# Performance work log

Hardware: AMD Instinct MI355X
Metric: run time of the kernel (lower is better)

The kernel has to match this reference:

```python
import jax, jax.numpy as jnp
import numpy as np

H = 1024          # hidden_size
NE = 16           # num_experts
GS = 4            # group_size (experts sharing a down projection)
DFF = int(H * 4 * 2 / 3)  # 2730, int(hidden*ffn_dim_multiplier*ffn_ratio)
BATCH, SEQ = 4, 2048
BS = BATCH * SEQ  # 8192 flattened tokens


def setup_inputs() -> dict:
    key = jax.random.key(0)
    k1, k2, k3, k4 = jax.random.split(key, 4)
    return {
        "x": jax.random.normal(k1, (BS, H), dtype=jnp.float32),
        "router_w": jax.random.normal(k2, (H, NE), dtype=jnp.float32) * 0.02,
        "router_b": jnp.zeros((NE,), dtype=jnp.float32),
        "up_w": jax.random.normal(k3, (NE, H, DFF), dtype=jnp.float32) * 0.02,
        "up_b": jnp.zeros((NE, DFF), dtype=jnp.float32),
        "down_w": jax.random.normal(k4, (NE // GS, DFF, H), dtype=jnp.float32) * 0.02,
        "down_b": jnp.zeros((NE // GS, H), dtype=jnp.float32),
        "batch_size": BATCH,
        "seq_len": SEQ,
    }


def reference(x, router_w, router_b, up_w, up_b, down_w, down_b, batch_size, seq_len):
    bs, hidden = x.shape
    num_experts = router_w.shape[1]
    # expert-choice capacity: k = bs * c // num_experts with c = 1.0
    k = bs // num_experts

    # linear router
    h_logits = x @ router_w + router_b          # [bs, E]
    S = jax.nn.softmax(h_logits, axis=-1)       # [bs, E]

    # each expert picks its top-k tokens (torch.topk(S, k, dim=0))
    G, idx = jax.lax.top_k(S.T, k)               # G: [E, k], idx: [E, k]

    # dispatch: einsum('bs k e, bs h -> e k h', P, x) == gather of chosen tokens
    tokens = x[idx]                              # [E, k, H]

    # grouped per-expert FFN: experts in a group share the down projection
    group_size = num_experts // down_w.shape[0]
    dw = jnp.repeat(down_w, group_size, axis=0)  # [E, DFF, H]
    db = jnp.repeat(down_b, group_size, axis=0)  # [E, H]

    hid = jax.nn.silu(jnp.einsum('ekh,ehd->ekd', tokens, up_w) + up_b[:, None, :])
    E_out = jnp.einsum('ekd,edh->ekh', hid, dw) + db[:, None, :]  # [E, k, H]

    # combine: einsum('bs k e, k e, e k h -> bs h', P, G, E) == weighted scatter-add
    weighted = G[:, :, None] * E_out             # [E, k, H]
    y = jnp.zeros_like(x).at[idx.reshape(-1)].add(weighted.reshape(-1, hidden))
    return y
```

## Files before the change

kernel.cpp:

```cpp
#include <hip/hip_runtime.h>
#include <stdint.h>

#define H 1024
#define NE 16
#define DFF 2730
#define DFFP 2752
#define DFFT 2816
#define BS 8192
#define KSEL 512
#define LDSP 40

typedef unsigned short u16;
typedef __attribute__((ext_vector_type(8))) short short8;
typedef __attribute__((ext_vector_type(4))) float f32x4;

__device__ __forceinline__ u16 f2b(float f) {
  unsigned u = __float_as_uint(f);
  unsigned r = (u + 0x7fffu + ((u >> 16) & 1u)) >> 16;
  return (u16)r;
}

__global__ __launch_bounds__(256) void zero_kernel(f32x4* __restrict__ out) {
  size_t i = ((size_t)blockIdx.x * 256 + threadIdx.x) * 2;
  f32x4 z = {0.f, 0.f, 0.f, 0.f};
  out[i] = z; out[i + 1] = z;
}

__global__ __launch_bounds__(256) void transcvt_kernel(
    const float* __restrict__ src, u16* __restrict__ dst,
    int Ks, int Ns, int Kd, long src_z, long dst_z) {
  src += (size_t)blockIdx.z * src_z;
  dst += (size_t)blockIdx.z * dst_z;
  __shared__ float t[32][33];
  int k0 = blockIdx.x * 32, n0 = blockIdx.y * 32;
  int r = threadIdx.x >> 3, c4 = (threadIdx.x & 7) * 4;
  int k = k0 + r;
#pragma unroll
  for (int j = 0; j < 4; ++j) {
    int n = n0 + c4 + j;
    t[r][c4 + j] = (k < Ks && n < Ns) ? src[(size_t)k * Ns + n] : 0.f;
  }
  __syncthreads();
  u16 o[4];
#pragma unroll
  for (int j = 0; j < 4; ++j) o[j] = f2b(t[c4 + j][r]);
  *(uint2*)&dst[(size_t)(n0 + r) * Kd + k0 + c4] = *(uint2*)o;
}

__global__ __launch_bounds__(256) void router_kernel(
    const float* __restrict__ x, const float* __restrict__ rw,
    const float* __restrict__ rb, double* __restrict__ S64, float* __restrict__ S32) {
  int w = threadIdx.x >> 6, lane = threadIdx.x & 63;
  int t = blockIdx.x * 4 + w;
  __shared__ double part[4][64][17];
  double acc[NE];
#pragma unroll
  for (int e = 0; e < NE; ++e) acc[e] = 0.0;
  const float* xr = x + (size_t)t * H + lane * 16;
  f32x4 xv[4];
#pragma unroll
  for (int q = 0; q < 4; ++q) xv[q] = *(const f32x4*)(xr + q * 4);
#pragma unroll
  for (int hh = 0; hh < 16; ++hh) {
    double xf = (double)xv[hh >> 2][hh & 3];
    const float* rwr = rw + (size_t)(lane * 16 + hh) * NE;
    f32x4 wv0 = *(const f32x4*)rwr;
    f32x4 wv1 = *(const f32x4*)(rwr + 4);
    f32x4 wv2 = *(const f32x4*)(rwr + 8);
    f32x4 wv3 = *(const f32x4*)(rwr + 12);
#pragma unroll
    for (int e = 0; e < 4; ++e) acc[e]      += xf * (double)wv0[e];
#pragma unroll
    for (int e = 0; e < 4; ++e) acc[4 + e]  += xf * (double)wv1[e];
#pragma unroll
    for (int e = 0; e < 4; ++e) acc[8 + e]  += xf * (double)wv2[e];
#pragma unroll
    for (int e = 0; e < 4; ++e) acc[12 + e] += xf * (double)wv3[e];
  }
#pragma unroll
  for (int e = 0; e < NE; ++e) part[w][lane][e] = acc[e];
  __syncthreads();
  if (lane < NE) {
    double s = (double)rb[lane];
#pragma unroll 8
    for (int r = 0; r < 64; ++r) s += part[w][r][lane];
    double m = s;
    for (int o = 8; o > 0; o >>= 1) m = fmax(m, __shfl_xor(m, o, 16));
    double ex = exp(s - m);
    double sum = ex;
    for (int o = 8; o > 0; o >>= 1) sum += __shfl_xor(sum, o, 16);
    double Sv = ex / sum;
    S64[(size_t)lane * BS + t] = Sv;
    S32[(size_t)lane * BS + t] = (float)Sv;
  }
}

__global__ __launch_bounds__(256) void topk_kernel(
    const float* __restrict__ S32, const double* __restrict__ S64,
    int* __restrict__ sel, float* __restrict__ gates) {
  int e = blockIdx.x, tid = threadIdx.x;
  __shared__ float sv[BS];
  __shared__ int red[4];
  __shared__ int cnt_s, gt_s, tie_cnt;
  __shared__ int tie_idx[256];
  const float* row = S32 + (size_t)e * BS;
  for (int i = tid; i < BS; i += 256) sv[i] = row[i];
  if (tid == 0) tie_cnt = 0;
  __syncthreads();
  unsigned thr = 0;
  for (int bit = 31; bit >= 0; --bit) {
    unsigned cand = thr | (1u << bit);
    int c = 0;
    for (int i = tid; i < BS; i += 256) c += (__float_as_uint(sv[i]) >= cand) ? 1 : 0;
#pragma unroll
    for (int o = 32; o > 0; o >>= 1) c += __shfl_down(c, o);
    if ((tid & 63) == 0) red[tid >> 6] = c;
    __syncthreads();
    if (tid == 0) cnt_s = red[0] + red[1] + red[2] + red[3];
    __syncthreads();
    if (cnt_s >= KSEL) thr = cand;
    __syncthreads();
  }
  {
    int c = 0;
    for (int i = tid; i < BS; i += 256) c += (__float_as_uint(sv[i]) > thr) ? 1 : 0;
#pragma unroll
    for (int o = 32; o > 0; o >>= 1) c += __shfl_down(c, o);
    if ((tid & 63) == 0) red[tid >> 6] = c;
    __syncthreads();
    if (tid == 0) gt_s = red[0] + red[1] + red[2] + red[3];
    __syncthreads();
  }
  int gt = gt_s;
  if (tid < 64) {
    int lane = tid, pos = 0;
    for (int c = 0; c < BS / 64; ++c) {
      int i = c * 64 + lane;
      bool p = __float_as_uint(sv[i]) > thr;
      unsigned long long b = __ballot(p);
      int rank = __popcll(b & ((1ull << lane) - 1ull));
      if (p) { sel[e * KSEL + pos + rank] = i; gates[e * KSEL + pos + rank] = sv[i]; }
      pos += __popcll(b);
    }
  }
  for (int i = tid; i < BS; i += 256) {
    if (__float_as_uint(sv[i]) == thr) {
      int p = atomicAdd(&tie_cnt, 1);
      if (p < 256) tie_idx[p] = i;
    }
  }
  __syncthreads();
  int T = tie_cnt < 256 ? tie_cnt : 256;
  int R = KSEL - gt;
  if (tid < T) {
    int i = tie_idx[tid];
    double vi = S64[(size_t)e * BS + i];
    int rank = 0;
    for (int j = 0; j < T; ++j) {
      if (j == tid) continue;
      int kdx = tie_idx[j];
      double vj = S64[(size_t)e * BS + kdx];
      rank += (vj > vi || (vj == vi && kdx < i)) ? 1 : 0;
    }
    if (rank < R) {
      sel[e * KSEL + gt + rank] = i;
      gates[e * KSEL + gt + rank] = sv[i];
    }
  }
}

__global__ __launch_bounds__(256) void up_gemm_kernel(
    const float* __restrict__ x, const int* __restrict__ sel,
    const u16* __restrict__ upT, const float* __restrict__ up_b,
    u16* __restrict__ hid, int e_base) {
  int nt = blockIdx.x;
  int mt = blockIdx.y;
  int z = blockIdx.z;
  int e = e_base + z;
  const u16* upTz = upT + (size_t)z * DFFT * H;
  u16* hidz = hid + (size_t)z * KSEL * DFFP;
  int tid = threadIdx.x, lane = tid & 63, w = tid >> 6;
  int wm = (w >> 1) * 64, wn = (w & 1) * 64;
  int n0 = nt * 128, m0 = mt * 128;
  __shared__ u16 As[128][LDSP];
  __shared__ u16 Bs[128][LDSP];
  __shared__ int sel_s[128];
  if (tid < 128) sel_s[tid] = sel[e * KSEL + m0 + tid];
  f32x4 zero = {0.f, 0.f, 0.f, 0.f};
  f32x4 acc[4][4];
#pragma unroll
  for (int i = 0; i < 4; ++i)
#pragma unroll
    for (int j = 0; j < 4; ++j) acc[i][j] = zero;
  int bn = tid & 127, bq = tid >> 7;
  const u16* brow = upTz + (size_t)(n0 + bn) * H + bq * 16;
  int arow = tid >> 1, ahalf = tid & 1;
  __syncthreads();
  const float* xrow = x + (size_t)sel_s[arow] * H + ahalf * 16;
  for (int k0 = 0; k0 < H; k0 += 32) {
    const float* ap = xrow + k0;
    f32x4 a0 = *(const f32x4*)ap;
    f32x4 a1 = *(const f32x4*)(ap + 4);
    f32x4 a2 = *(const f32x4*)(ap + 8);
    f32x4 a3 = *(const f32x4*)(ap + 12);
    short8 pa0, pa1;
#pragma unroll
    for (int q = 0; q < 4; ++q) { pa0[q] = (short)f2b(a0[q]); pa0[4 + q] = (short)f2b(a1[q]); }
#pragma unroll
    for (int q = 0; q < 4; ++q) { pa1[q] = (short)f2b(a2[q]); pa1[4 + q] = (short)f2b(a3[q]); }
    short8 qb0 = *(const short8*)(brow + k0);
    short8 qb1 = *(const short8*)(brow + k0 + 8);
    __syncthreads();
    *(short8*)&As[arow][ahalf * 16] = pa0;
    *(short8*)&As[arow][ahalf * 16 + 8] = pa1;
    *(short8*)&Bs[bn][bq * 16] = qb0;
    *(short8*)&Bs[bn][bq * 16 + 8] = qb1;
    __syncthreads();
    int lm = lane & 15, lk = (lane >> 4) * 8;
    short8 af[4], bfr[4];
#pragma unroll
    for (int i = 0; i < 4; ++i) af[i] = *(short8*)&As[wm + i * 16 + lm][lk];
#pragma unroll
    for (int j = 0; j < 4; ++j) bfr[j] = *(short8*)&Bs[wn + j * 16 + lm][lk];
#pragma unroll
    for (int i = 0; i < 4; ++i)
#pragma unroll
      for (int j = 0; j < 4; ++j)
        acc[i][j] = __builtin_amdgcn_mfma_f32_16x16x32_bf16(af[i], bfr[j], acc[i][j], 0, 0, 0);
  }
  int lm = lane & 15, q = lane >> 4;
#pragma unroll
  for (int i = 0; i < 4; ++i) {
#pragma unroll
    for (int j = 0; j < 4; ++j) {
      int col = n0 + wn + j * 16 + lm;
      if (col >= DFFP) continue;
      float bias = (col < DFF) ? up_b[(size_t)e * DFF + col] : 0.f;
#pragma unroll
      for (int r = 0; r < 4; ++r) {
        int rowl = m0 + wm + i * 16 + q * 4 + r;
        float v = acc[i][j][r] + bias;
        v = v / (1.f + __expf(-v));
        hidz[(size_t)rowl * DFFP + col] = f2b(v);
      }
    }
  }
}

__global__ __launch_bounds__(256) void down_gemm_kernel(
    const u16* __restrict__ hid, const u16* __restrict__ dwT,
    const float* __restrict__ db, const int* __restrict__ selp,
    const float* __restrict__ gatesp, float* __restrict__ out) {
  int nt = blockIdx.x;
  int mt = blockIdx.y;
  int z = blockIdx.z;
  const u16* hidz = hid + (size_t)z * 2048 * DFFP;
  const u16* dwTz = dwT + (size_t)z * H * DFFP;
  const float* dbz = db + (size_t)z * H;
  const int* selz = selp + z * 2048;
  const float* gatesz = gatesp + z * 2048;
  int tid = threadIdx.x, lane = tid & 63, w = tid >> 6;
  int wm = (w >> 1) * 64, wn = (w & 1) * 64;
  int n0 = nt * 128, m0 = mt * 128;
  __shared__ u16 As[128][LDSP];
  __shared__ u16 Bs[128][LDSP];
  __shared__ int sel_s[128];
  __shared__ float gate_s[128];
  if (tid < 128) {
    sel_s[tid] = selz[m0 + tid];
    gate_s[tid] = gatesz[m0 + tid];
  }
  f32x4 zero = {0.f, 0.f, 0.f, 0.f};
  f32x4 acc[4][4];
#pragma unroll
  for (int i = 0; i < 4; ++i)
#pragma unroll
    for (int j = 0; j < 4; ++j) acc[i][j] = zero;
  int bn = tid & 127, bq = tid >> 7;
  const u16* brow = dwTz + (size_t)(n0 + bn) * DFFP + bq * 16;
  int arow0 = tid >> 2, akv = tid & 3;
  __syncthreads();
  for (int k0 = 0; k0 < DFFP; k0 += 32) {
    short8 av0 = *(const short8*)(hidz + (size_t)(m0 + arow0) * DFFP + k0 + akv * 8);
    short8 av1 = *(const short8*)(hidz + (size_t)(m0 + arow0 + 64) * DFFP + k0 + akv * 8);
    short8 qb0 = *(const short8*)(brow + k0);
    short8 qb1 = *(const short8*)(brow + k0 + 8);
    __syncthreads();
    *(short8*)&As[arow0][akv * 8] = av0;
    *(short8*)&As[arow0 + 64][akv * 8] = av1;
    *(short8*)&Bs[bn][bq * 16] = qb0;
    *(short8*)&Bs[bn][bq * 16 + 8] = qb1;
    __syncthreads();
    int lm = lane & 15, lk = (lane >> 4) * 8;
    short8 af[4], bfr[4];
#pragma unroll
    for (int i = 0; i < 4; ++i) af[i] = *(short8*)&As[wm + i * 16 + lm][lk];
#pragma unroll
    for (int j = 0; j < 4; ++j) bfr[j] = *(short8*)&Bs[wn + j * 16 + lm][lk];
#pragma unroll
    for (int i = 0; i < 4; ++i)
#pragma unroll
      for (int j = 0; j < 4; ++j)
        acc[i][j] = __builtin_amdgcn_mfma_f32_16x16x32_bf16(af[i], bfr[j], acc[i][j], 0, 0, 0);
  }
  int lm = lane & 15, q = lane >> 4;
#pragma unroll
  for (int i = 0; i < 4; ++i) {
#pragma unroll
    for (int j = 0; j < 4; ++j) {
      int col = n0 + wn + j * 16 + lm;
      float bias = dbz[col];
#pragma unroll
      for (int r = 0; r < 4; ++r) {
        int rowl = wm + i * 16 + q * 4 + r;
        float v = (acc[i][j][r] + bias) * gate_s[rowl];
        atomicAdd(&out[(size_t)sel_s[rowl] * H + col], v);
      }
    }
  }
}

extern "C" void kernel_launch(void* const* d_in, const int* in_sizes, int n_in,
                              void* d_out, int out_size, void* d_ws, size_t ws_size,
                              hipStream_t stream) {
  const float* x      = (const float*)d_in[0];
  const float* rw     = (const float*)d_in[1];
  const float* rb     = (const float*)d_in[2];
  const float* up_w   = (const float*)d_in[3];
  const float* up_b   = (const float*)d_in[4];
  const float* down_w = (const float*)d_in[5];
  const float* down_b = (const float*)d_in[6];
  char* ws = (char*)d_ws;
  double* S64  = (double*)ws;
  float*  S32  = (float*)(ws + 1048576);
  int*    sel  = (int*)(ws + 1572864);
  float*  gates= (float*)(ws + 1605632);
  const size_t base = 1638400;

  const size_t upT_e  = (size_t)DFFT * H * 2;
  const size_t dwT_g  = (size_t)H * DFFP * 2;
  const size_t hid_e  = (size_t)KSEL * DFFP * 2;

  size_t need16 = base + 16 * upT_e + 4 * dwT_g + 16 * hid_e;
  size_t need4  = base + 4 * upT_e + 1 * dwT_g + 4 * hid_e;
  int cs = (ws_size >= need16) ? 16 : (ws_size >= need4 ? 4 : 1);

  float* outf = (float*)d_out;
  zero_kernel<<<BS * H / 8 / 256, 256, 0, stream>>>((f32x4*)d_out);
  router_kernel<<<BS / 4, 256, 0, stream>>>(x, rw, rb, S64, S32);
  topk_kernel<<<NE, 256, 0, stream>>>(S32, S64, sel, gates);

  if (cs == 16) {
    u16* upT = (u16*)(ws + base);
    u16* dwT = (u16*)(ws + base + 16 * upT_e);
    u16* hid = (u16*)(ws + base + 16 * upT_e + 4 * dwT_g);
    transcvt_kernel<<<dim3(H / 32, DFFT / 32, 16), 256, 0, stream>>>(
        up_w, upT, H, DFF, H, (long)H * DFF, (long)DFFT * H);
    transcvt_kernel<<<dim3(DFFP / 32, H / 32, 4), 256, 0, stream>>>(
        down_w, dwT, DFF, H, DFFP, (long)DFF * H, (long)H * DFFP);
    up_gemm_kernel<<<dim3(22, 4, 16), 256, 0, stream>>>(x, sel, upT, up_b, hid, 0);
    down_gemm_kernel<<<dim3(8, 16, 4), 256, 0, stream>>>(hid, dwT, down_b, sel, gates, outf);
  } else if (cs == 4) {
    u16* upT = (u16*)(ws + base);
    u16* dwT = (u16*)(ws + base + 4 * upT_e);
    u16* hid = (u16*)(ws + base + 4 * upT_e + dwT_g);
    for (int g = 0; g < 4; ++g) {
      transcvt_kernel<<<dim3(H / 32, DFFT / 32, 4), 256, 0, stream>>>(
          up_w + (size_t)g * 4 * H * DFF, upT, H, DFF, H, (long)H * DFF, (long)DFFT * H);
      transcvt_kernel<<<dim3(DFFP / 32, H / 32, 1), 256, 0, stream>>>(
          down_w + (size_t)g * DFF * H, dwT, DFF, H, DFFP, 0, 0);
      up_gemm_kernel<<<dim3(22, 4, 4), 256, 0, stream>>>(x, sel, upT, up_b, hid, g * 4);
      down_gemm_kernel<<<dim3(8, 16, 1), 256, 0, stream>>>(
          hid, dwT, down_b + g * H, sel + g * 2048, gates + g * 2048, outf);
    }
  } else {
    u16* upT = (u16*)(ws + base);
    u16* dwT = (u16*)(ws + base + upT_e);
    u16* hid = (u16*)(ws + base + upT_e + dwT_g);
    for (int e = 0; e < 16; ++e) {
      transcvt_kernel<<<dim3(H / 32, DFFT / 32, 1), 256, 0, stream>>>(
          up_w + (size_t)e * H * DFF, upT, H, DFF, H, 0, 0);
      transcvt_kernel<<<dim3(DFFP / 32, H / 32, 1), 256, 0, stream>>>(
          down_w + (size_t)(e >> 2) * DFF * H, dwT, DFF, H, DFFP, 0, 0);
      up_gemm_kernel<<<dim3(22, 4, 1), 256, 0, stream>>>(x, sel, upT, up_b, hid, e);
      down_gemm_kernel<<<dim3(8, 4, 1), 256, 0, stream>>>(
          hid, dwT, down_b + (e >> 2) * H, sel + e * KSEL, gates + e * KSEL, outf);
    }
  }
}
```

Measured before the change: 705.6 us.

## Pre-gather bf16 tokens and load GEMM tiles directly to LDS with swizzle

Adds a gather kernel that converts the selected token rows to bf16 once, so the up GEMM no longer re-reads and re-converts fp32 x for every N tile. Both GEMMs now fill shared memory with global_load_lds, store tiles unpadded with an XOR swizzle to avoid bank conflicts, and swap the grid axes so blocks sharing a weight tile launch together. This cuts register staging and redundant conversion, but costs an extra launch and workspace for the gathered tokens, and the loop still uses single-buffered loads with two barriers per step.

```diff
diff --git a/kernel.cpp b/kernel.cpp
--- a/kernel.cpp
+++ b/kernel.cpp
@@ -8,7 +8,6 @@
 #define DFFT 2816
 #define BS 8192
 #define KSEL 512
-#define LDSP 40
 
 typedef unsigned short u16;
 typedef __attribute__((ext_vector_type(8))) short short8;
@@ -18,6 +17,12 @@
   unsigned u = __float_as_uint(f);
   unsigned r = (u + 0x7fffu + ((u >> 16) & 1u)) >> 16;
   return (u16)r;
+}
+
+typedef const __attribute__((address_space(1))) unsigned int* gas_t;
+typedef __attribute__((address_space(3))) unsigned int* las_t;
+__device__ __forceinline__ void gload16(const u16* g, u16* l) {
+  __builtin_amdgcn_global_load_lds((gas_t)g, (las_t)l, 16, 0, 0);
 }
 
 __global__ __launch_bounds__(256) void zero_kernel(f32x4* __restrict__ out) {
@@ -45,6 +50,17 @@
 #pragma unroll
   for (int j = 0; j < 4; ++j) o[j] = f2b(t[c4 + j][r]);
   *(uint2*)&dst[(size_t)(n0 + r) * Kd + k0 + c4] = *(uint2*)o;
+}
+
+__global__ __launch_bounds__(256) void gather_kernel(
+    const float* __restrict__ x, const int* __restrict__ sel, u16* __restrict__ xg) {
+  int row = blockIdx.x;
+  const float* src = x + (size_t)sel[row] * H + threadIdx.x * 4;
+  f32x4 v = *(const f32x4*)src;
+  u16 o[4];
+#pragma unroll
+  for (int j = 0; j < 4; ++j) o[j] = f2b(v[j]);
+  *(uint2*)&xg[(size_t)row * H + threadIdx.x * 4] = *(uint2*)o;
 }
 
 __global__ __launch_bounds__(256) void router_kernel(
@@ -169,66 +185,61 @@
   }
 }
 
+
 __global__ __launch_bounds__(256) void up_gemm_kernel(
-    const float* __restrict__ x, const int* __restrict__ sel,
-    const u16* __restrict__ upT, const float* __restrict__ up_b,
-    u16* __restrict__ hid, int e_base) {
-  int nt = blockIdx.x;
-  int mt = blockIdx.y;
+    const u16* __restrict__ xg, const u16* __restrict__ upT,
+    const float* __restrict__ up_b, u16* __restrict__ hid, int e_base) {
+  int mt = blockIdx.x;
+  int nt = blockIdx.y;
   int z = blockIdx.z;
   int e = e_base + z;
-  const u16* upTz = upT + (size_t)z * DFFT * H;
+  const u16* Abase = xg + (size_t)z * KSEL * H + (size_t)(mt * 128) * H;
+  const u16* Bbase = upT + (size_t)z * DFFT * H + (size_t)(nt * 128) * H;
   u16* hidz = hid + (size_t)z * KSEL * DFFP;
   int tid = threadIdx.x, lane = tid & 63, w = tid >> 6;
   int wm = (w >> 1) * 64, wn = (w & 1) * 64;
   int n0 = nt * 128, m0 = mt * 128;
-  __shared__ u16 As[128][LDSP];
-  __shared__ u16 Bs[128][LDSP];
-  __shared__ int sel_s[128];
-  if (tid < 128) sel_s[tid] = sel[e * KSEL + m0 + tid];
+  __shared__ __align__(16) u16 As[128 * 32];
+  __shared__ __align__(16) u16 Bs[128 * 32];
+  int r0 = tid >> 2, cg0 = (tid & 3) ^ ((r0 >> 1) & 3);
+  const u16* pa0 = Abase + (size_t)r0 * H + cg0 * 8;
+  const u16* pa1 = Abase + (size_t)(r0 + 64) * H + cg0 * 8;
+  const u16* pb0 = Bbase + (size_t)r0 * H + cg0 * 8;
+  const u16* pb1 = Bbase + (size_t)(r0 + 64) * H + cg0 * 8;
+  u16* la0 = As + tid * 8;  u16* la1 = As + 2048 + tid * 8;
+  u16* lb0 = Bs + tid * 8;  u16* lb1 = Bs + 2048 + tid * 8;
   f32x4 zero = {0.f, 0.f, 0.f, 0.f};
   f32x4 acc[4][4];
 #pragma unroll
   for (int i = 0; i < 4; ++i)
 #pragma unroll
     for (int j = 0; j < 4; ++j) acc[i][j] = zero;
-  int bn = tid & 127, bq = tid >> 7;
-  const u16* brow = upTz + (size_t)(n0 + bn) * H + bq * 16;
-  int arow = tid >> 1, ahalf = tid & 1;
-  __syncthreads();
-  const float* xrow = x + (size_t)sel_s[arow] * H + ahalf * 16;
+  int lm = lane & 15, g = lane >> 4;
   for (int k0 = 0; k0 < H; k0 += 32) {
-    const float* ap = xrow + k0;
-    f32x4 a0 = *(const f32x4*)ap;
-    f32x4 a1 = *(const f32x4*)(ap + 4);
-    f32x4 a2 = *(const f32x4*)(ap + 8);
-    f32x4 a3 = *(const f32x4*)(ap + 12);
-    short8 pa0, pa1;
-#pragma unroll
-    for (int q = 0; q < 4; ++q) { pa0[q] = (short)f2b(a0[q]); pa0[4 + q] = (short)f2b(a1[q]); }
-#pragma unroll
-    for (int q = 0; q < 4; ++q) { pa1[q] = (short)f2b(a2[q]); pa1[4 + q] = (short)f2b(a3[q]); }
-    short8 qb0 = *(const short8*)(brow + k0);
-    short8 qb1 = *(const short8*)(brow + k0 + 8);
-    __syncthreads();
-    *(short8*)&As[arow][ahalf * 16] = pa0;
-    *(short8*)&As[arow][ahalf * 16 + 8] = pa1;
-    *(short8*)&Bs[bn][bq * 16] = qb0;
-    *(short8*)&Bs[bn][bq * 16 + 8] = qb1;
-    __syncthreads();
-    int lm = lane & 15, lk = (lane >> 4) * 8;
+    gload16(pa0 + k0, la0);
+    gload16(pa1 + k0, la1);
+    gload16(pb0 + k0, lb0);
+    gload16(pb1 + k0, lb1);
+    __syncthreads();
     short8 af[4], bfr[4];
 #pragma unroll
-    for (int i = 0; i < 4; ++i) af[i] = *(short8*)&As[wm + i * 16 + lm][lk];
-#pragma unroll
-    for (int j = 0; j < 4; ++j) bfr[j] = *(short8*)&Bs[wn + j * 16 + lm][lk];
+    for (int i = 0; i < 4; ++i) {
+      int row = wm + i * 16 + lm;
+      af[i] = *(short8*)&As[row * 32 + ((g ^ ((row >> 1) & 3)) * 8)];
+    }
+#pragma unroll
+    for (int j = 0; j < 4; ++j) {
+      int row = wn + j * 16 + lm;
+      bfr[j] = *(short8*)&Bs[row * 32 + ((g ^ ((row >> 1) & 3)) * 8)];
+    }
 #pragma unroll
     for (int i = 0; i < 4; ++i)
 #pragma unroll
       for (int j = 0; j < 4; ++j)
         acc[i][j] = __builtin_amdgcn_mfma_f32_16x16x32_bf16(af[i], bfr[j], acc[i][j], 0, 0, 0);
-  }
-  int lm = lane & 15, q = lane >> 4;
+    __syncthreads();
+  }
+  int q = lane >> 4;
 #pragma unroll
   for (int i = 0; i < 4; ++i) {
 #pragma unroll
@@ -251,59 +262,63 @@
     const u16* __restrict__ hid, const u16* __restrict__ dwT,
     const float* __restrict__ db, const int* __restrict__ selp,
     const float* __restrict__ gatesp, float* __restrict__ out) {
-  int nt = blockIdx.x;
-  int mt = blockIdx.y;
+  int mt = blockIdx.x;
+  int nt = blockIdx.y;
   int z = blockIdx.z;
-  const u16* hidz = hid + (size_t)z * 2048 * DFFP;
-  const u16* dwTz = dwT + (size_t)z * H * DFFP;
+  const u16* Abase = hid + (size_t)z * 2048 * DFFP + (size_t)(mt * 128) * DFFP;
+  const u16* Bbase = dwT + (size_t)z * H * DFFP + (size_t)(nt * 128) * DFFP;
   const float* dbz = db + (size_t)z * H;
-  const int* selz = selp + z * 2048;
-  const float* gatesz = gatesp + z * 2048;
   int tid = threadIdx.x, lane = tid & 63, w = tid >> 6;
   int wm = (w >> 1) * 64, wn = (w & 1) * 64;
   int n0 = nt * 128, m0 = mt * 128;
-  __shared__ u16 As[128][LDSP];
-  __shared__ u16 Bs[128][LDSP];
+  __shared__ __align__(16) u16 As[128 * 32];
+  __shared__ __align__(16) u16 Bs[128 * 32];
   __shared__ int sel_s[128];
   __shared__ float gate_s[128];
   if (tid < 128) {
-    sel_s[tid] = selz[m0 + tid];
-    gate_s[tid] = gatesz[m0 + tid];
-  }
+    sel_s[tid] = selp[z * 2048 + m0 + tid];
+    gate_s[tid] = gatesp[z * 2048 + m0 + tid];
+  }
+  int r0 = tid >> 2, cg0 = (tid & 3) ^ ((r0 >> 1) & 3);
+  const u16* pa0 = Abase + (size_t)r0 * DFFP + cg0 * 8;
+  const u16* pa1 = Abase + (size_t)(r0 + 64) * DFFP + cg0 * 8;
+  const u16* pb0 = Bbase + (size_t)r0 * DFFP + cg0 * 8;
+  const u16* pb1 = Bbase + (size_t)(r0 + 64) * DFFP + cg0 * 8;
+  u16* la0 = As + tid * 8;  u16* la1 = As + 2048 + tid * 8;
+  u16* lb0 = Bs + tid * 8;  u16* lb1 = Bs + 2048 + tid * 8;
   f32x4 zero = {0.f, 0.f, 0.f, 0.f};
   f32x4 acc[4][4];
 #pragma unroll
   for (int i = 0; i < 4; ++i)
 #pragma unroll
     for (int j = 0; j < 4; ++j) acc[i][j] = zero;
-  int bn = tid & 127, bq = tid >> 7;
-  const u16* brow = dwTz + (size_t)(n0 + bn) * DFFP + bq * 16;
-  int arow0 = tid >> 2, akv = tid & 3;
+  int lm = lane & 15, g = lane >> 4;
   __syncthreads();
   for (int k0 = 0; k0 < DFFP; k0 += 32) {
-    short8 av0 = *(const short8*)(hidz + (size_t)(m0 + arow0) * DFFP + k0 + akv * 8);
-    short8 av1 = *(const short8*)(hidz + (size_t)(m0 + arow0 + 64) * DFFP + k0 + akv * 8);
-    short8 qb0 = *(const short8*)(brow + k0);
-    short8 qb1 = *(const short8*)(brow + k0 + 8);
-    __syncthreads();
-    *(short8*)&As[arow0][akv * 8] = av0;
-    *(short8*)&As[arow0 + 64][akv * 8] = av1;
-    *(short8*)&Bs[bn][bq * 16] = qb0;
-    *(short8*)&Bs[bn][bq * 16 + 8] = qb1;
-    __syncthreads();
-    int lm = lane & 15, lk = (lane >> 4) * 8;
+    gload16(pa0 + k0, la0);
+    gload16(pa1 + k0, la1);
+    gload16(pb0 + k0, lb0);
+    gload16(pb1 + k0, lb1);
+    __syncthreads();
     short8 af[4], bfr[4];
 #pragma unroll
-    for (int i = 0; i < 4; ++i) af[i] = *(short8*)&As[wm + i * 16 + lm][lk];
-#pragma unroll
-    for (int j = 0; j < 4; ++j) bfr[j] = *(short8*)&Bs[wn + j * 16 + lm][lk];
+    for (int i = 0; i < 4; ++i) {
+      int row = wm + i * 16 + lm;
+      af[i] = *(short8*)&As[row * 32 + ((g ^ ((row >> 1) & 3)) * 8)];
+    }
+#pragma unroll
+    for (int j = 0; j < 4; ++j) {
+      int row = wn + j * 16 + lm;
+      bfr[j] = *(short8*)&Bs[row * 32 + ((g ^ ((row >> 1) & 3)) * 8)];
+    }
 #pragma unroll
     for (int i = 0; i < 4; ++i)
 #pragma unroll
       for (int j = 0; j < 4; ++j)
         acc[i][j] = __builtin_amdgcn_mfma_f32_16x16x32_bf16(af[i], bfr[j], acc[i][j], 0, 0, 0);
-  }
-  int lm = lane & 15, q = lane >> 4;
+    __syncthreads();
+  }
+  int q = lane >> 4;
 #pragma unroll
   for (int i = 0; i < 4; ++i) {
 #pragma unroll
@@ -340,9 +355,10 @@
   const size_t upT_e  = (size_t)DFFT * H * 2;
   const size_t dwT_g  = (size_t)H * DFFP * 2;
   const size_t hid_e  = (size_t)KSEL * DFFP * 2;
-
-  size_t need16 = base + 16 * upT_e + 4 * dwT_g + 16 * hid_e;
-  size_t need4  = base + 4 * upT_e + 1 * dwT_g + 4 * hid_e;
+  const size_t xg_e   = (size_t)KSEL * H * 2;
+
+  size_t need16 = base + 16 * upT_e + 4 * dwT_g + 16 * hid_e + 16 * xg_e;
+  size_t need4  = base + 4 * upT_e + 1 * dwT_g + 4 * hid_e + 4 * xg_e;
   int cs = (ws_size >= need16) ? 16 : (ws_size >= need4 ? 4 : 1);
 
   float* outf = (float*)d_out;
@@ -354,36 +370,42 @@
     u16* upT = (u16*)(ws + base);
     u16* dwT = (u16*)(ws + base + 16 * upT_e);
     u16* hid = (u16*)(ws + base + 16 * upT_e + 4 * dwT_g);
+    u16* xg  = (u16*)(ws + base + 16 * upT_e + 4 * dwT_g + 16 * hid_e);
     transcvt_kernel<<<dim3(H / 32, DFFT / 32, 16), 256, 0, stream>>>(
         up_w, upT, H, DFF, H, (long)H * DFF, (long)DFFT * H);
     transcvt_kernel<<<dim3(DFFP / 32, H / 32, 4), 256, 0, stream>>>(
         down_w, dwT, DFF, H, DFFP, (long)DFF * H, (long)H * DFFP);
-    up_gemm_kernel<<<dim3(22, 4, 16), 256, 0, stream>>>(x, sel, upT, up_b, hid, 0);
-    down_gemm_kernel<<<dim3(8, 16, 4), 256, 0, stream>>>(hid, dwT, down_b, sel, gates, outf);
+    gather_kernel<<<NE * KSEL, 256, 0, stream>>>(x, sel, xg);
+    up_gemm_kernel<<<dim3(4, 22, 16), 256, 0, stream>>>(xg, upT, up_b, hid, 0);
+    down_gemm_kernel<<<dim3(16, 8, 4), 256, 0, stream>>>(hid, dwT, down_b, sel, gates, outf);
   } else if (cs == 4) {
     u16* upT = (u16*)(ws + base);
     u16* dwT = (u16*)(ws + base + 4 * upT_e);
     u16* hid = (u16*)(ws + base + 4 * upT_e + dwT_g);
+    u16* xg  = (u16*)(ws + base + 4 * upT_e + dwT_g + 4 * hid_e);
     for (int g = 0; g < 4; ++g) {
       transcvt_kernel<<<dim3(H / 32, DFFT / 32, 4), 256, 0, stream>>>(
           up_w + (size_t)g * 4 * H * DFF, upT, H, DFF, H, (long)H * DFF, (long)DFFT * H);
       transcvt_kernel<<<dim3(DFFP / 32, H / 32, 1), 256, 0, stream>>>(
           down_w + (size_t)g * DFF * H, dwT, DFF, H, DFFP, 0, 0);
-      up_gemm_kernel<<<dim3(22, 4, 4), 256, 0, stream>>>(x, sel, upT, up_b, hid, g * 4);
-      down_gemm_kernel<<<dim3(8, 16, 1), 256, 0, stream>>>(
+      gather_kernel<<<4 * KSEL, 256, 0, stream>>>(x, sel + g * 2048, xg);
+      up_gemm_kernel<<<dim3(4, 22, 4), 256, 0, stream>>>(xg, upT, up_b, hid, g * 4);
+      down_gemm_kernel<<<dim3(16, 8, 1), 256, 0, stream>>>(
           hid, dwT, down_b + g * H, sel + g * 2048, gates + g * 2048, outf);
     }
   } else {
     u16* upT = (u16*)(ws + base);
     u16* dwT = (u16*)(ws + base + upT_e);
     u16* hid = (u16*)(ws + base + upT_e + dwT_g);
+    u16* xg  = (u16*)(ws + base + upT_e + dwT_g + hid_e);
     for (int e = 0; e < 16; ++e) {
       transcvt_kernel<<<dim3(H / 32, DFFT / 32, 1), 256, 0, stream>>>(
           up_w + (size_t)e * H * DFF, upT, H, DFF, H, 0, 0);
       transcvt_kernel<<<dim3(DFFP / 32, H / 32, 1), 256, 0, stream>>>(
           down_w + (size_t)(e >> 2) * DFF * H, dwT, DFF, H, DFFP, 0, 0);
-      up_gemm_kernel<<<dim3(22, 4, 1), 256, 0, stream>>>(x, sel, upT, up_b, hid, e);
-      down_gemm_kernel<<<dim3(8, 4, 1), 256, 0, stream>>>(
+      gather_kernel<<<KSEL, 256, 0, stream>>>(x, sel + e * KSEL, xg);
+      up_gemm_kernel<<<dim3(4, 22, 1), 256, 0, stream>>>(xg, upT, up_b, hid, e);
+      down_gemm_kernel<<<dim3(4, 8, 1), 256, 0, stream>>>(
           hid, dwT, down_b + (e >> 2) * H, sel + e * KSEL, gates + e * KSEL, outf);
     }
   }
```

Measured after the change: 637.8 us. 9.6% less time.
